# Kernel optimization log

Measured on AMD Instinct MI355X. Metric: run time of the kernel, lower is better.

Reference implementation:

```python
import jax, jax.numpy as jnp
import numpy as np

D_MODEL, D_STATE, D_CONV, EXPAND, L = 512, 16, 4, 2, 2048
D_INNER = EXPAND * D_MODEL


def _dwconv_causal(x, w, b):
    # x: (L, D), w: (D, K), b: (D,). torch Conv1d(groups=D, padding=K-1)[..., :L]
    K = w.shape[1]
    xp = jnp.pad(x, ((K - 1, 0), (0, 0)))
    windows = jnp.stack([xp[k:k + x.shape[0]] for k in range(K)], axis=-1)  # (L, D, K)
    return jnp.einsum('ldk,dk->ld', windows, w) + b


def _ssm_dir(x, inW, inb, cw, cb, xpW, xpb, dtW, dtb, outW, outb, A_log, Dp):
    xz = x @ inW + inb                      # (L, 2*Di)
    x_ssm, z = xz[:, :D_INNER], xz[:, D_INNER:]
    x_ssm = _dwconv_causal(x_ssm, cw, cb)   # (L, Di)
    sp = jax.nn.silu(x_ssm) @ xpW + xpb     # (L, Di + 2*S)
    delta = sp[:, :D_INNER]
    B = sp[:, D_INNER:D_INNER + D_STATE]
    C = sp[:, D_INNER + D_STATE:]
    dt = jax.nn.softplus(delta @ dtW + dtb)  # (L, Di)
    A = -jnp.exp(A_log)                      # (Di, S)
    dA = jnp.exp(dt[:, :, None] * A[None])                      # (L, Di, S)
    dBu = dt[:, :, None] * B[:, None, :] * x_ssm[:, :, None]    # (L, Di, S)

    def step(h, inp):
        a, bu = inp
        h = a * h + bu
        return h, h

    h0 = jnp.zeros((D_INNER, D_STATE), x.dtype)
    _, hs = jax.lax.scan(step, h0, (dA, dBu))   # (L, Di, S)
    y = jnp.einsum('lds,ls->ld', hs, C) + Dp * x_ssm
    return (y * jax.nn.silu(z)) @ outW + outb


def _make_params(key):
    ks = jax.random.split(key, 32)
    i = iter(range(32))
    def w(shape, scale=0.02):
        return (jax.random.normal(ks[next(i)], shape, jnp.float32) * scale)
    p = {}
    for pre in ('fwd_', 'bwd_'):
        p[pre + 'in_W'] = w((D_MODEL, 2 * D_INNER))
        p[pre + 'in_b'] = w((2 * D_INNER,))
        p[pre + 'conv_w'] = w((D_INNER, D_CONV), 0.1)
        p[pre + 'conv_b'] = w((D_INNER,))
        p[pre + 'xp_W'] = w((D_INNER, D_INNER + 2 * D_STATE))
        p[pre + 'xp_b'] = w((D_INNER + 2 * D_STATE,))
        p[pre + 'dt_W'] = w((D_INNER, D_INNER))
        p[pre + 'dt_b'] = w((D_INNER,))
        p[pre + 'out_W'] = w((D_INNER, D_MODEL))
        p[pre + 'out_b'] = w((D_MODEL,))
    p['A_log'] = jax.random.normal(ks[next(i)], (D_INNER, D_STATE), jnp.float32) * 0.5
    p['D_param'] = jnp.ones((D_INNER,), jnp.float32)
    p['fusion_W'] = w((2 * D_MODEL, D_MODEL))
    p['fusion_b'] = w((D_MODEL,))
    return p


def setup_inputs() -> dict:
    key = jax.random.key(0)
    kx, kp = jax.random.split(key)
    inp = {'x': jax.random.normal(kx, (L, D_MODEL), jnp.float32)}
    inp.update(_make_params(kp))
    return inp


def reference(x,
              fwd_in_W, fwd_in_b, fwd_conv_w, fwd_conv_b, fwd_xp_W, fwd_xp_b,
              fwd_dt_W, fwd_dt_b, fwd_out_W, fwd_out_b,
              bwd_in_W, bwd_in_b, bwd_conv_w, bwd_conv_b, bwd_xp_W, bwd_xp_b,
              bwd_dt_W, bwd_dt_b, bwd_out_W, bwd_out_b,
              A_log, D_param, fusion_W, fusion_b):
    out_fwd = _ssm_dir(x, fwd_in_W, fwd_in_b, fwd_conv_w, fwd_conv_b,
                       fwd_xp_W, fwd_xp_b, fwd_dt_W, fwd_dt_b,
                       fwd_out_W, fwd_out_b, A_log, D_param)
    out_bwd = _ssm_dir(x[::-1], bwd_in_W, bwd_in_b, bwd_conv_w, bwd_conv_b,
                       bwd_xp_W, bwd_xp_b, bwd_dt_W, bwd_dt_b,
                       bwd_out_W, bwd_out_b, A_log, D_param)[::-1]
    return jnp.concatenate([out_fwd, out_bwd], axis=-1) @ fusion_W + fusion_b
```

## Files before the change

kernel.cpp:

```cpp
#include <hip/hip_runtime.h>
#include <cmath>

#define L_SEQ 2048
#define DM 512
#define DI 1024
#define DS 16
#define NSP 1056
#define NC 64
#define CL 32

typedef unsigned short ushortT;
typedef unsigned int u32;
typedef __attribute__((ext_vector_type(8))) short short8;
typedef __attribute__((ext_vector_type(4))) float float4_t;
typedef __attribute__((address_space(1))) u32 gu32;
typedef __attribute__((address_space(3))) u32 lu32;

__device__ __forceinline__ float sigm(float x) { return 1.0f / (1.0f + __expf(-x)); }

__device__ __forceinline__ ushortT f2bf(float f) {
    unsigned u = __float_as_uint(f);
    unsigned r = u + 0x7FFFu + ((u >> 16) & 1u);
    return (ushortT)(r >> 16);
}

__device__ __forceinline__ void gl2lds16(const ushortT* g, ushortT* l) {
    __builtin_amdgcn_global_load_lds((gu32*)g, (lu32*)l, 16, 0, 0);
}

struct WC {
    const float* src[9];
    ushortT* dst[9];
    int K[9], N[9], tN[9];
    int off[10];
};

__global__ __launch_bounds__(256) void wcvt_all(WC wc)
{
    __shared__ ushortT t[32][33];
    int b = blockIdx.x;
    int m = 0;
    while (b >= wc.off[m + 1]) ++m;
    int tl = b - wc.off[m];
    int n0 = (tl % wc.tN[m]) * 32;
    int k0 = (tl / wc.tN[m]) * 32;
    const float* W = wc.src[m];
    ushortT* Wt = wc.dst[m];
    int K = wc.K[m], N = wc.N[m];
    int tx = threadIdx.x & 31, ty = threadIdx.x >> 5;
    #pragma unroll
    for (int i = 0; i < 32; i += 8)
        t[ty + i][tx] = f2bf(W[(size_t)(k0 + ty + i) * N + n0 + tx]);
    __syncthreads();
    #pragma unroll
    for (int i = 0; i < 32; i += 8)
        Wt[(size_t)(n0 + ty + i) * K + k0 + tx] = t[tx][ty + i];
}

__global__ __launch_bounds__(256) void xcvt_k(const float* __restrict__ x,
                                              ushortT* __restrict__ xb, int n)
{
    int i = (blockIdx.x * 256 + threadIdx.x) * 4;
    if (i < n) {
        float4_t v = *(const float4_t*)(x + i);
        xb[i + 0] = f2bf(v[0]); xb[i + 1] = f2bf(v[1]);
        xb[i + 2] = f2bf(v[2]); xb[i + 3] = f2bf(v[3]);
    }
}

template<int BM, int BN>
__global__ __launch_bounds__(256, 2) void gemm_bf16(
    const ushortT* __restrict__ A, int lda, long long Astr, int revAmode,
    const ushortT* __restrict__ W, long long Wstr,
    const float* __restrict__ bias0, const float* __restrict__ bias1,
    float* __restrict__ Cf, int ldcf, long long Cfstr,
    ushortT* __restrict__ Cb, int ldcb, long long Cbstr, int Nbmax,
    int revCmode, int M, int N, int K, int epi)
{
    const int dir = blockIdx.z;
    A  += (size_t)dir * Astr;
    W  += (size_t)dir * Wstr;
    if (Cf) Cf += (size_t)dir * Cfstr;
    if (Cb) Cb += (size_t)dir * Cbstr;
    const float* bias = dir ? bias1 : bias0;
    const int revA = (revAmode == 2) ? dir : revAmode;
    const int revC = (revCmode == 2) ? dir : revCmode;

    constexpr int MI = BM / 32;
    constexpr int NI = BN / 32;
    constexpr int CA = BM / 64;
    constexpr int CB = BN / 64;

    __shared__ ushortT As[2][BM * 32];
    __shared__ ushortT Bs[2][BN * 32];

    const int tid  = threadIdx.x;
    const int wave = tid >> 6;
    const int lane = tid & 63;
    const int quad = lane >> 4;
    const int r    = lane & 15;
    const int wm   = (wave >> 1) * (BM / 2);
    const int wn   = (wave & 1) * (BN / 2);
    const int bm   = blockIdx.y * BM;
    const int bn   = blockIdx.x * BN;

    const int lrow = lane >> 2;
    const int lk   = (lane & 3) * 8;

    const ushortT* gA[CA];
    ushortT* lA[CA];
    #pragma unroll
    for (int c = 0; c < CA; ++c) {
        int row = bm + c * 64 + wave * 16 + lrow;
        if (revA) row = M - 1 - row;
        gA[c] = A + (size_t)row * lda + lk;
        lA[c] = &As[0][(c * 64 + wave * 16) * 32];
    }
    const ushortT* gB[CB];
    ushortT* lB[CB];
    #pragma unroll
    for (int c = 0; c < CB; ++c) {
        int row = bn + c * 64 + wave * 16 + lrow;
        if (row > N - 1) row = N - 1;
        gB[c] = W + (size_t)row * K + lk;
        lB[c] = &Bs[0][(c * 64 + wave * 16) * 32];
    }
    constexpr int ABUF = BM * 32;
    constexpr int BBUF = BN * 32;

    float4_t acc[MI][NI];
    #pragma unroll
    for (int i = 0; i < MI; ++i)
        #pragma unroll
        for (int j = 0; j < NI; ++j)
            acc[i][j] = (float4_t){0.f, 0.f, 0.f, 0.f};

    const int nsteps = K >> 5;

    #pragma unroll
    for (int c = 0; c < CA; ++c) gl2lds16(gA[c], lA[c]);
    #pragma unroll
    for (int c = 0; c < CB; ++c) gl2lds16(gB[c], lB[c]);

    for (int i = 0; i < nsteps; i += 2) {
        __syncthreads();
        {
            int kq = (i + 1) << 5;
            if (i + 1 < nsteps) {
                #pragma unroll
                for (int c = 0; c < CA; ++c) gl2lds16(gA[c] + kq, lA[c] + ABUF);
                #pragma unroll
                for (int c = 0; c < CB; ++c) gl2lds16(gB[c] + kq, lB[c] + BBUF);
            }
        }
        {
            short8 af[MI], bf[NI];
            #pragma unroll
            for (int mi = 0; mi < MI; ++mi)
                af[mi] = *(const short8*)&As[0][(wm + mi * 16 + r) * 32 + quad * 8];
            #pragma unroll
            for (int ni = 0; ni < NI; ++ni)
                bf[ni] = *(const short8*)&Bs[0][(wn + ni * 16 + r) * 32 + quad * 8];
            #pragma unroll
            for (int mi = 0; mi < MI; ++mi)
                #pragma unroll
                for (int ni = 0; ni < NI; ++ni)
                    acc[mi][ni] = __builtin_amdgcn_mfma_f32_16x16x32_bf16(
                        af[mi], bf[ni], acc[mi][ni], 0, 0, 0);
        }
        __syncthreads();
        {
            int kq = (i + 2) << 5;
            if (i + 2 < nsteps) {
                #pragma unroll
                for (int c = 0; c < CA; ++c) gl2lds16(gA[c] + kq, lA[c]);
                #pragma unroll
                for (int c = 0; c < CB; ++c) gl2lds16(gB[c] + kq, lB[c]);
            }
        }
        {
            short8 af[MI], bf[NI];
            #pragma unroll
            for (int mi = 0; mi < MI; ++mi)
                af[mi] = *(const short8*)&As[1][(wm + mi * 16 + r) * 32 + quad * 8];
            #pragma unroll
            for (int ni = 0; ni < NI; ++ni)
                bf[ni] = *(const short8*)&Bs[1][(wn + ni * 16 + r) * 32 + quad * 8];
            #pragma unroll
            for (int mi = 0; mi < MI; ++mi)
                #pragma unroll
                for (int ni = 0; ni < NI; ++ni)
                    acc[mi][ni] = __builtin_amdgcn_mfma_f32_16x16x32_bf16(
                        af[mi], bf[ni], acc[mi][ni], 0, 0, 0);
        }
    }

    #pragma unroll
    for (int mi = 0; mi < MI; ++mi) {
        int rowb = bm + wm + mi * 16 + quad * 4;
        #pragma unroll
        for (int ni = 0; ni < NI; ++ni) {
            int gn = bn + wn + ni * 16 + r;
            if (gn < N) {
                float bv = bias[gn];
                #pragma unroll
                for (int j = 0; j < 4; ++j) {
                    int orow = rowb + j;
                    if (revC) orow = M - 1 - orow;
                    float v = acc[mi][ni][j] + bv;
                    if (epi == 1) v = (v > 20.0f) ? v : log1pf(__expf(v));
                    if (Cf) Cf[(size_t)orow * ldcf + gn] = v;
                    if (Cb && gn < Nbmax) Cb[(size_t)orow * ldcb + gn] = f2bf(v);
                }
            }
        }
    }
}

__global__ __launch_bounds__(256) void conv_k(
    const float* __restrict__ XZ,
    const float* __restrict__ cw0, const float* __restrict__ cw1,
    const float* __restrict__ cb0, const float* __restrict__ cb1,
    float* __restrict__ XC, ushortT* __restrict__ SCb)
{
    int dir = blockIdx.z;
    XZ += (size_t)dir * L_SEQ * 2 * DI;
    XC += (size_t)dir * L_SEQ * DI;
    SCb += (size_t)dir * L_SEQ * DI;
    const float* cw = dir ? cw1 : cw0;
    const float* cb = dir ? cb1 : cb0;
    int idx = blockIdx.x * 256 + threadIdx.x;
    int d = idx & (DI - 1);
    int l = idx >> 10;
    float w0 = cw[d * 4 + 0], w1 = cw[d * 4 + 1], w2 = cw[d * 4 + 2], w3 = cw[d * 4 + 3];
    float acc = cb[d];
    if (l >= 3) acc += XZ[(size_t)(l - 3) * (2 * DI) + d] * w0;
    if (l >= 2) acc += XZ[(size_t)(l - 2) * (2 * DI) + d] * w1;
    if (l >= 1) acc += XZ[(size_t)(l - 1) * (2 * DI) + d] * w2;
    acc += XZ[(size_t)l * (2 * DI) + d] * w3;
    XC[idx] = acc;
    SCb[idx] = f2bf(acc * sigm(acc));
}

__global__ __launch_bounds__(256) void scanA_k(
    const float* __restrict__ DT, const float* __restrict__ XC,
    const float* __restrict__ SP, const float* __restrict__ Alog,
    float* __restrict__ Pend, float* __restrict__ Hl)
{
    __shared__ float Bsh[CL][DS];
    int dir = blockIdx.z;
    int c = blockIdx.y;
    int d = blockIdx.x * 256 + threadIdx.x;
    DT += (size_t)dir * L_SEQ * DI;
    XC += (size_t)dir * L_SEQ * DI;
    SP += (size_t)dir * L_SEQ * NSP;
    int l0 = c * CL;
    for (int i = threadIdx.x; i < CL * DS; i += 256) {
        int ll = i >> 4, ss = i & 15;
        Bsh[ll][ss] = SP[(size_t)(l0 + ll) * NSP + DI + ss];
    }
    __syncthreads();
    float Ae[DS], h[DS], P[DS];
    #pragma unroll
    for (int s = 0; s < DS; ++s) { Ae[s] = -__expf(Alog[d * DS + s]); h[s] = 0.f; P[s] = 1.f; }
    for (int t = 0; t < CL; ++t) {
        int l = l0 + t;
        float dt = DT[(size_t)l * DI + d];
        float xv = XC[(size_t)l * DI + d];
        float dtx = dt * xv;
        #pragma unroll
        for (int s = 0; s < DS; ++s) {
            float e = __expf(dt * Ae[s]);
            h[s] = e * h[s] + dtx * Bsh[t][s];
            P[s] *= e;
        }
    }
    size_t o = ((size_t)(dir * NC + c) * DI + d) * DS;
    #pragma unroll
    for (int s = 0; s < DS; ++s) { Pend[o + s] = P[s]; Hl[o + s] = h[s]; }
}

__global__ __launch_bounds__(256) void scanB_k(
    const float* __restrict__ Pend, const float* __restrict__ Hl, float* __restrict__ Hs)
{
    int idx = blockIdx.x * 256 + threadIdx.x;
    float h = 0.f;
    int ds = idx & 16383;
    int dir = idx >> 14;
    for (int c = 0; c < NC; ++c) {
        size_t o = ((size_t)(dir * NC + c)) * (DI * DS) + ds;
        Hs[o] = h;
        h = Pend[o] * h + Hl[o];
    }
}

__global__ __launch_bounds__(256) void scanC_k(
    const float* __restrict__ DT, const float* __restrict__ XC,
    const float* __restrict__ SP, const float* __restrict__ XZ,
    const float* __restrict__ Alog, const float* __restrict__ Dp,
    const float* __restrict__ Hs, ushortT* __restrict__ Gb)
{
    __shared__ float Bsh[CL][DS];
    __shared__ float Csh[CL][DS];
    int dir = blockIdx.z;
    int c = blockIdx.y;
    int d = blockIdx.x * 256 + threadIdx.x;
    DT += (size_t)dir * L_SEQ * DI;
    XC += (size_t)dir * L_SEQ * DI;
    SP += (size_t)dir * L_SEQ * NSP;
    XZ += (size_t)dir * L_SEQ * (2 * DI);
    Gb += (size_t)dir * L_SEQ * DI;
    int l0 = c * CL;
    for (int i = threadIdx.x; i < CL * DS; i += 256) {
        int ll = i >> 4, ss = i & 15;
        size_t base = (size_t)(l0 + ll) * NSP + DI;
        Bsh[ll][ss] = SP[base + ss];
        Csh[ll][ss] = SP[base + DS + ss];
    }
    __syncthreads();
    float Ae[DS], h[DS];
    size_t o = ((size_t)(dir * NC + c) * DI + d) * DS;
    #pragma unroll
    for (int s = 0; s < DS; ++s) { Ae[s] = -__expf(Alog[d * DS + s]); h[s] = Hs[o + s]; }
    float dpv = Dp[d];
    for (int t = 0; t < CL; ++t) {
        int l = l0 + t;
        float dt = DT[(size_t)l * DI + d];
        float xv = XC[(size_t)l * DI + d];
        float dtx = dt * xv;
        float y = 0.f;
        #pragma unroll
        for (int s = 0; s < DS; ++s) {
            float e = __expf(dt * Ae[s]);
            h[s] = e * h[s] + dtx * Bsh[t][s];
            y += h[s] * Csh[t][s];
        }
        y += dpv * xv;
        float z = XZ[(size_t)l * (2 * DI) + DI + d];
        Gb[(size_t)l * DI + d] = f2bf(y * (z * sigm(z)));
    }
}

extern "C" void kernel_launch(void* const* d_in, const int* in_sizes, int n_in,
                              void* d_out, int out_size, void* d_ws, size_t ws_size,
                              hipStream_t stream)
{
    (void)in_sizes; (void)n_in; (void)out_size; (void)ws_size;
    const float* x = (const float*)d_in[0];
    const float* inW[2]  = {(const float*)d_in[1],  (const float*)d_in[11]};
    const float* inb[2]  = {(const float*)d_in[2],  (const float*)d_in[12]};
    const float* cw[2]   = {(const float*)d_in[3],  (const float*)d_in[13]};
    const float* cb[2]   = {(const float*)d_in[4],  (const float*)d_in[14]};
    const float* xpW[2]  = {(const float*)d_in[5],  (const float*)d_in[15]};
    const float* xpb[2]  = {(const float*)d_in[6],  (const float*)d_in[16]};
    const float* dtW[2]  = {(const float*)d_in[7],  (const float*)d_in[17]};
    const float* dtb[2]  = {(const float*)d_in[8],  (const float*)d_in[18]};
    const float* outW[2] = {(const float*)d_in[9],  (const float*)d_in[19]};
    const float* outb[2] = {(const float*)d_in[10], (const float*)d_in[20]};
    const float* Alog = (const float*)d_in[21];
    const float* Dp   = (const float*)d_in[22];
    const float* fuW  = (const float*)d_in[23];
    const float* fub  = (const float*)d_in[24];
    float* out = (float*)d_out;

    float* ws = (float*)d_ws;
    size_t off = 0;
    auto alloc = [&](size_t n) { float* p = ws + off; off += n; return p; };
    float* XZ  = alloc((size_t)2 * L_SEQ * 2 * DI);
    float* XC  = alloc((size_t)2 * L_SEQ * DI);
    float* SP  = alloc((size_t)2 * L_SEQ * NSP);
    float* DTb = alloc((size_t)2 * L_SEQ * DI);
    float* Pend= alloc((size_t)2 * NC * DI * DS);
    float* Hl  = alloc((size_t)2 * NC * DI * DS);
    float* Hs  = alloc((size_t)2 * NC * DI * DS);

    ushortT* wsu = (ushortT*)(ws + off);
    size_t uoff = 0;
    auto ualloc = [&](size_t n) { ushortT* p = wsu + uoff; uoff += n; return p; };
    ushortT* WtIn  = ualloc((size_t)2 * (2 * DI) * DM);
    ushortT* WtXp  = ualloc((size_t)2 * NSP * DI);
    ushortT* WtDt  = ualloc((size_t)2 * DI * DI);
    ushortT* WtOut = ualloc((size_t)2 * DM * DI);
    ushortT* WtFu  = ualloc((size_t)DM * DI);
    ushortT* XB    = ualloc((size_t)L_SEQ * DM);
    ushortT* SCb   = ualloc((size_t)2 * L_SEQ * DI);
    ushortT* SPb   = ualloc((size_t)2 * L_SEQ * DI);
    ushortT* Gb    = ualloc((size_t)2 * L_SEQ * DI);
    ushortT* OCb   = ualloc((size_t)L_SEQ * DI);

    dim3 blk(256);

    WC wc;
    const float* srcs[9] = {inW[0], inW[1], xpW[0], xpW[1], dtW[0], dtW[1],
                            outW[0], outW[1], fuW};
    ushortT* dsts[9] = {WtIn, WtIn + (size_t)2 * DI * DM,
                        WtXp, WtXp + (size_t)NSP * DI,
                        WtDt, WtDt + (size_t)DI * DI,
                        WtOut, WtOut + (size_t)DM * DI,
                        WtFu};
    int Ks[9] = {DM, DM, DI, DI, DI, DI, DI, DI, DI};
    int Ns[9] = {2 * DI, 2 * DI, NSP, NSP, DI, DI, DM, DM, DM};
    wc.off[0] = 0;
    for (int m = 0; m < 9; ++m) {
        wc.src[m] = srcs[m]; wc.dst[m] = dsts[m];
        wc.K[m] = Ks[m]; wc.N[m] = Ns[m];
        wc.tN[m] = Ns[m] / 32;
        wc.off[m + 1] = wc.off[m] + (Ns[m] / 32) * (Ks[m] / 32);
    }
    wcvt_all<<<dim3(wc.off[9]), blk, 0, stream>>>(wc);
    xcvt_k<<<dim3(L_SEQ * DM / 1024), blk, 0, stream>>>(x, XB, L_SEQ * DM);

    gemm_bf16<128, 128><<<dim3(16, 16, 2), blk, 0, stream>>>(
        XB, DM, 0, 2, WtIn, (long long)2 * DI * DM, inb[0], inb[1],
        XZ, 2 * DI, (long long)L_SEQ * 2 * DI, nullptr, 0, 0, 0,
        0, L_SEQ, 2 * DI, DM, 0);
    conv_k<<<dim3(L_SEQ * DI / 256, 1, 2), blk, 0, stream>>>(
        XZ, cw[0], cw[1], cb[0], cb[1], XC, SCb);
    gemm_bf16<128, 64><<<dim3((NSP + 63) / 64, 16, 2), blk, 0, stream>>>(
        SCb, DI, (long long)L_SEQ * DI, 0, WtXp, (long long)NSP * DI, xpb[0], xpb[1],
        SP, NSP, (long long)L_SEQ * NSP, SPb, DI, (long long)L_SEQ * DI, DI,
        0, L_SEQ, NSP, DI, 0);
    gemm_bf16<128, 64><<<dim3(16, 16, 2), blk, 0, stream>>>(
        SPb, DI, (long long)L_SEQ * DI, 0, WtDt, (long long)DI * DI, dtb[0], dtb[1],
        DTb, DI, (long long)L_SEQ * DI, nullptr, 0, 0, 0,
        0, L_SEQ, DI, DI, 1);
    scanA_k<<<dim3(DI / 256, NC, 2), blk, 0, stream>>>(DTb, XC, SP, Alog, Pend, Hl);
    scanB_k<<<dim3(2 * DI * DS / 256), blk, 0, stream>>>(Pend, Hl, Hs);
    scanC_k<<<dim3(DI / 256, NC, 2), blk, 0, stream>>>(DTb, XC, SP, XZ, Alog, Dp, Hs, Gb);
    gemm_bf16<64, 64><<<dim3(8, 32, 2), blk, 0, stream>>>(
        Gb, DI, (long long)L_SEQ * DI, 0, WtOut, (long long)DM * DI, outb[0], outb[1],
        nullptr, 0, 0, OCb, DI, (long long)DM, DM,
        2, L_SEQ, DM, DI, 0);
    gemm_bf16<64, 64><<<dim3(8, 32, 1), blk, 0, stream>>>(
        OCb, DI, 0, 0, WtFu, 0, fub, fub,
        out, DM, (long long)0, nullptr, 0, 0, 0,
        0, L_SEQ, DM, DI, 0);
}
```

Measured before the change: 346.8 us.

## Fold xp→dt and out→fusion weight products into precomputed combined GEMMs

Precomputes fused weight matrices (xp_W[:, :Di] @ dt_W, and out_W @ fusion_W halves) with small on-device GEMMs, plus folded biases. The separate dt projection GEMM and the fusion GEMM are removed from the main path: a single GEMM now produces softplus(dt) and B/C together, and the out projection accumulates both directions straight into the output with atomics after a memset. This cuts two large activation GEMMs and intermediate buffers, at the cost of extra weight-prep GEMMs per call, atomic contention, and altered bf16 rounding of combined weights. Tile sizes also change for the input GEMM and launch bounds are relaxed.

```diff
diff --git a/kernel.cpp b/kernel.cpp
--- a/kernel.cpp
+++ b/kernel.cpp
@@ -29,10 +29,10 @@
 }
 
 struct WC {
-    const float* src[9];
-    ushortT* dst[9];
-    int K[9], N[9], tN[9];
-    int off[10];
+    const float* src[11];
+    ushortT* dst[11];
+    int ss[11], soff[11], ds_[11], tN[11], mode[11];
+    int off[12];
 };
 
 __global__ __launch_bounds__(256) void wcvt_all(WC wc)
@@ -45,16 +45,55 @@
     int n0 = (tl % wc.tN[m]) * 32;
     int k0 = (tl / wc.tN[m]) * 32;
     const float* W = wc.src[m];
-    ushortT* Wt = wc.dst[m];
-    int K = wc.K[m], N = wc.N[m];
+    ushortT* D = wc.dst[m];
+    int ss = wc.ss[m], soff = wc.soff[m], ds = wc.ds_[m];
     int tx = threadIdx.x & 31, ty = threadIdx.x >> 5;
-    #pragma unroll
-    for (int i = 0; i < 32; i += 8)
-        t[ty + i][tx] = f2bf(W[(size_t)(k0 + ty + i) * N + n0 + tx]);
-    __syncthreads();
-    #pragma unroll
-    for (int i = 0; i < 32; i += 8)
-        Wt[(size_t)(n0 + ty + i) * K + k0 + tx] = t[tx][ty + i];
+    if (wc.mode[m] == 1) {
+        #pragma unroll
+        for (int i = 0; i < 32; i += 8)
+            D[(size_t)(k0 + ty + i) * ds + n0 + tx] =
+                f2bf(W[(size_t)(k0 + ty + i) * ss + soff + n0 + tx]);
+    } else {
+        #pragma unroll
+        for (int i = 0; i < 32; i += 8)
+            t[ty + i][tx] = f2bf(W[(size_t)(k0 + ty + i) * ss + soff + n0 + tx]);
+        __syncthreads();
+        #pragma unroll
+        for (int i = 0; i < 32; i += 8)
+            D[(size_t)(n0 + ty + i) * ds + k0 + tx] = t[tx][ty + i];
+    }
+}
+
+__global__ __launch_bounds__(256) void bias_fold(
+    const float* __restrict__ xpb0, const float* __restrict__ xpb1,
+    const float* __restrict__ dtW0, const float* __restrict__ dtW1,
+    const float* __restrict__ dtb0, const float* __restrict__ dtb1,
+    const float* __restrict__ outb0, const float* __restrict__ outb1,
+    const float* __restrict__ fuW, const float* __restrict__ fub,
+    float* __restrict__ BFdt0, float* __restrict__ BFdt1, float* __restrict__ BFof)
+{
+    int idx = blockIdx.x * 256 + threadIdx.x;
+    if (idx < 2112) {
+        int dir = idx >= 1056;
+        int m = idx - dir * 1056;
+        const float* xpb = dir ? xpb1 : xpb0;
+        float* BF = dir ? BFdt1 : BFdt0;
+        if (m < 1024) {
+            const float* dtW = dir ? dtW1 : dtW0;
+            const float* dtb = dir ? dtb1 : dtb0;
+            float acc = dtb[m];
+            for (int n = 0; n < 1024; ++n) acc += xpb[n] * dtW[n * 1024 + m];
+            BF[m] = acc;
+        } else {
+            BF[m] = xpb[m];
+        }
+    } else if (idx < 2624) {
+        int n = idx - 2112;
+        float acc = fub[n];
+        for (int j = 0; j < 512; ++j)  acc += outb0[j] * fuW[j * 512 + n];
+        for (int j = 0; j < 512; ++j)  acc += outb1[j] * fuW[(512 + j) * 512 + n];
+        BFof[n] = acc;
+    }
 }
 
 __global__ __launch_bounds__(256) void xcvt_k(const float* __restrict__ x,
@@ -69,22 +108,23 @@
 }
 
 template<int BM, int BN>
-__global__ __launch_bounds__(256, 2) void gemm_bf16(
+__global__ __launch_bounds__(256) void gemm_bf16(
     const ushortT* __restrict__ A, int lda, long long Astr, int revAmode,
     const ushortT* __restrict__ W, long long Wstr,
     const float* __restrict__ bias0, const float* __restrict__ bias1,
     float* __restrict__ Cf, int ldcf, long long Cfstr,
-    ushortT* __restrict__ Cb, int ldcb, long long Cbstr, int Nbmax,
-    int revCmode, int M, int N, int K, int epi)
+    float* __restrict__ Cf2, int ldcf2, long long Cf2str, int Nsplit,
+    ushortT* __restrict__ Cb, int ldcb, long long Cbstr,
+    int M, int N, int K, int epi)
 {
     const int dir = blockIdx.z;
     A  += (size_t)dir * Astr;
     W  += (size_t)dir * Wstr;
-    if (Cf) Cf += (size_t)dir * Cfstr;
-    if (Cb) Cb += (size_t)dir * Cbstr;
+    if (Cf)  Cf  += (size_t)dir * Cfstr;
+    if (Cf2) Cf2 += (size_t)dir * Cf2str;
+    if (Cb)  Cb  += (size_t)dir * Cbstr;
     const float* bias = dir ? bias1 : bias0;
     const int revA = (revAmode == 2) ? dir : revAmode;
-    const int revC = (revCmode == 2) ? dir : revCmode;
 
     constexpr int MI = BM / 32;
     constexpr int NI = BN / 32;
@@ -202,15 +242,22 @@
         for (int ni = 0; ni < NI; ++ni) {
             int gn = bn + wn + ni * 16 + r;
             if (gn < N) {
-                float bv = bias[gn];
+                float bv = bias ? bias[gn] : 0.0f;
                 #pragma unroll
                 for (int j = 0; j < 4; ++j) {
                     int orow = rowb + j;
-                    if (revC) orow = M - 1 - orow;
                     float v = acc[mi][ni][j] + bv;
-                    if (epi == 1) v = (v > 20.0f) ? v : log1pf(__expf(v));
-                    if (Cf) Cf[(size_t)orow * ldcf + gn] = v;
-                    if (Cb && gn < Nbmax) Cb[(size_t)orow * ldcb + gn] = f2bf(v);
+                    if (epi == 1 && gn < Nsplit) v = (v > 20.0f) ? v : log1pf(__expf(v));
+                    if (epi == 3) {
+                        atomicAdd(&Cf[(size_t)orow * ldcf + gn], v);
+                    } else {
+                        if (gn < Nsplit) {
+                            if (Cf) Cf[(size_t)orow * ldcf + gn] = v;
+                        } else if (Cf2) {
+                            Cf2[(size_t)orow * ldcf2 + gn - Nsplit] = v;
+                        }
+                        if (Cb) Cb[(size_t)orow * ldcb + gn] = f2bf(v);
+                    }
                 }
             }
         }
@@ -244,7 +291,7 @@
 
 __global__ __launch_bounds__(256) void scanA_k(
     const float* __restrict__ DT, const float* __restrict__ XC,
-    const float* __restrict__ SP, const float* __restrict__ Alog,
+    const float* __restrict__ BC, const float* __restrict__ Alog,
     float* __restrict__ Pend, float* __restrict__ Hl)
 {
     __shared__ float Bsh[CL][DS];
@@ -253,11 +300,11 @@
     int d = blockIdx.x * 256 + threadIdx.x;
     DT += (size_t)dir * L_SEQ * DI;
     XC += (size_t)dir * L_SEQ * DI;
-    SP += (size_t)dir * L_SEQ * NSP;
+    BC += (size_t)dir * L_SEQ * 32;
     int l0 = c * CL;
     for (int i = threadIdx.x; i < CL * DS; i += 256) {
         int ll = i >> 4, ss = i & 15;
-        Bsh[ll][ss] = SP[(size_t)(l0 + ll) * NSP + DI + ss];
+        Bsh[ll][ss] = BC[(size_t)(l0 + ll) * 32 + ss];
     }
     __syncthreads();
     float Ae[DS], h[DS], P[DS];
@@ -296,7 +343,7 @@
 
 __global__ __launch_bounds__(256) void scanC_k(
     const float* __restrict__ DT, const float* __restrict__ XC,
-    const float* __restrict__ SP, const float* __restrict__ XZ,
+    const float* __restrict__ BC, const float* __restrict__ XZ,
     const float* __restrict__ Alog, const float* __restrict__ Dp,
     const float* __restrict__ Hs, ushortT* __restrict__ Gb)
 {
@@ -307,15 +354,15 @@
     int d = blockIdx.x * 256 + threadIdx.x;
     DT += (size_t)dir * L_SEQ * DI;
     XC += (size_t)dir * L_SEQ * DI;
-    SP += (size_t)dir * L_SEQ * NSP;
+    BC += (size_t)dir * L_SEQ * 32;
     XZ += (size_t)dir * L_SEQ * (2 * DI);
     Gb += (size_t)dir * L_SEQ * DI;
     int l0 = c * CL;
     for (int i = threadIdx.x; i < CL * DS; i += 256) {
         int ll = i >> 4, ss = i & 15;
-        size_t base = (size_t)(l0 + ll) * NSP + DI;
-        Bsh[ll][ss] = SP[base + ss];
-        Csh[ll][ss] = SP[base + DS + ss];
+        size_t base = (size_t)(l0 + ll) * 32;
+        Bsh[ll][ss] = BC[base + ss];
+        Csh[ll][ss] = BC[base + DS + ss];
     }
     __syncthreads();
     float Ae[DS], h[DS];
@@ -366,73 +413,87 @@
     float* ws = (float*)d_ws;
     size_t off = 0;
     auto alloc = [&](size_t n) { float* p = ws + off; off += n; return p; };
-    float* XZ  = alloc((size_t)2 * L_SEQ * 2 * DI);
-    float* XC  = alloc((size_t)2 * L_SEQ * DI);
-    float* SP  = alloc((size_t)2 * L_SEQ * NSP);
-    float* DTb = alloc((size_t)2 * L_SEQ * DI);
-    float* Pend= alloc((size_t)2 * NC * DI * DS);
-    float* Hl  = alloc((size_t)2 * NC * DI * DS);
-    float* Hs  = alloc((size_t)2 * NC * DI * DS);
+    float* XZ   = alloc((size_t)2 * L_SEQ * 2 * DI);
+    float* XC   = alloc((size_t)2 * L_SEQ * DI);
+    float* DTb  = alloc((size_t)2 * L_SEQ * DI);
+    float* BCf  = alloc((size_t)2 * L_SEQ * 32);
+    float* Pend = alloc((size_t)2 * NC * DI * DS);
+    float* Hl   = alloc((size_t)2 * NC * DI * DS);
+    float* Hs   = alloc((size_t)2 * NC * DI * DS);
+    float* BFdt0 = alloc(1056);
+    float* BFdt1 = alloc(1056);
+    float* BFof  = alloc(512);
 
     ushortT* wsu = (ushortT*)(ws + off);
     size_t uoff = 0;
     auto ualloc = [&](size_t n) { ushortT* p = wsu + uoff; uoff += n; return p; };
     ushortT* WtIn  = ualloc((size_t)2 * (2 * DI) * DM);
-    ushortT* WtXp  = ualloc((size_t)2 * NSP * DI);
     ushortT* WtDt  = ualloc((size_t)2 * DI * DI);
-    ushortT* WtOut = ualloc((size_t)2 * DM * DI);
     ushortT* WtFu  = ualloc((size_t)DM * DI);
+    ushortT* WtXpF = ualloc((size_t)2 * NSP * DI);
+    ushortT* XpD   = ualloc((size_t)2 * DI * DI);
+    ushortT* OutC  = ualloc((size_t)2 * DI * DM);
+    ushortT* WtOF  = ualloc((size_t)2 * DM * DI);
     ushortT* XB    = ualloc((size_t)L_SEQ * DM);
     ushortT* SCb   = ualloc((size_t)2 * L_SEQ * DI);
-    ushortT* SPb   = ualloc((size_t)2 * L_SEQ * DI);
     ushortT* Gb    = ualloc((size_t)2 * L_SEQ * DI);
-    ushortT* OCb   = ualloc((size_t)L_SEQ * DI);
 
     dim3 blk(256);
 
+    hipMemsetAsync(out, 0, (size_t)L_SEQ * DM * sizeof(float), stream);
+
     WC wc;
-    const float* srcs[9] = {inW[0], inW[1], xpW[0], xpW[1], dtW[0], dtW[1],
-                            outW[0], outW[1], fuW};
-    ushortT* dsts[9] = {WtIn, WtIn + (size_t)2 * DI * DM,
-                        WtXp, WtXp + (size_t)NSP * DI,
-                        WtDt, WtDt + (size_t)DI * DI,
-                        WtOut, WtOut + (size_t)DM * DI,
-                        WtFu};
-    int Ks[9] = {DM, DM, DI, DI, DI, DI, DI, DI, DI};
-    int Ns[9] = {2 * DI, 2 * DI, NSP, NSP, DI, DI, DM, DM, DM};
+    struct E { const float* s; ushortT* d; int ss, so, ds, N, K, mode; };
+    E es[11] = {
+        {inW[0],  WtIn,                          2 * DI, 0,    DM, 2 * DI, DM, 0},
+        {inW[1],  WtIn + (size_t)2 * DI * DM,    2 * DI, 0,    DM, 2 * DI, DM, 0},
+        {dtW[0],  WtDt,                          DI,     0,    DI, DI,     DI, 0},
+        {dtW[1],  WtDt + (size_t)DI * DI,        DI,     0,    DI, DI,     DI, 0},
+        {fuW,     WtFu,                          DM,     0,    DI, DM,     DI, 0},
+        {xpW[0],  WtXpF + (size_t)DI * DI,       NSP,    DI,   DI, 32,     DI, 0},
+        {xpW[1],  WtXpF + (size_t)NSP * DI + (size_t)DI * DI, NSP, DI, DI, 32, DI, 0},
+        {xpW[0],  XpD,                           NSP,    0,    DI, DI,     DI, 1},
+        {xpW[1],  XpD + (size_t)DI * DI,         NSP,    0,    DI, DI,     DI, 1},
+        {outW[0], OutC,                          DM,     0,    DM, DM,     DI, 1},
+        {outW[1], OutC + (size_t)DI * DM,        DM,     0,    DM, DM,     DI, 1},
+    };
     wc.off[0] = 0;
-    for (int m = 0; m < 9; ++m) {
-        wc.src[m] = srcs[m]; wc.dst[m] = dsts[m];
-        wc.K[m] = Ks[m]; wc.N[m] = Ns[m];
-        wc.tN[m] = Ns[m] / 32;
-        wc.off[m + 1] = wc.off[m] + (Ns[m] / 32) * (Ks[m] / 32);
-    }
-    wcvt_all<<<dim3(wc.off[9]), blk, 0, stream>>>(wc);
+    for (int m = 0; m < 11; ++m) {
+        wc.src[m] = es[m].s; wc.dst[m] = es[m].d;
+        wc.ss[m] = es[m].ss; wc.soff[m] = es[m].so; wc.ds_[m] = es[m].ds;
+        wc.tN[m] = es[m].N / 32; wc.mode[m] = es[m].mode;
+        wc.off[m + 1] = wc.off[m] + (es[m].N / 32) * (es[m].K / 32);
+    }
+    wcvt_all<<<dim3(wc.off[11]), blk, 0, stream>>>(wc);
     xcvt_k<<<dim3(L_SEQ * DM / 1024), blk, 0, stream>>>(x, XB, L_SEQ * DM);
-
-    gemm_bf16<128, 128><<<dim3(16, 16, 2), blk, 0, stream>>>(
+    bias_fold<<<dim3(11), blk, 0, stream>>>(
+        xpb[0], xpb[1], dtW[0], dtW[1], dtb[0], dtb[1],
+        outb[0], outb[1], fuW, fub, BFdt0, BFdt1, BFof);
+
+    gemm_bf16<64, 64><<<dim3(16, 16, 2), blk, 0, stream>>>(
+        WtDt, DI, (long long)DI * DI, 0, XpD, (long long)DI * DI,
+        nullptr, nullptr, nullptr, 0, 0, nullptr, 0, 0, DI,
+        WtXpF, DI, (long long)NSP * DI, DI, DI, DI, 0);
+    gemm_bf16<64, 64><<<dim3(16, 8, 2), blk, 0, stream>>>(
+        WtFu, DI, (long long)DM, 0, OutC, (long long)DI * DM,
+        nullptr, nullptr, nullptr, 0, 0, nullptr, 0, 0, DI,
+        WtOF, DI, (long long)DM * DI, DM, DI, DM, 0);
+
+    gemm_bf16<64, 128><<<dim3(16, 32, 2), blk, 0, stream>>>(
         XB, DM, 0, 2, WtIn, (long long)2 * DI * DM, inb[0], inb[1],
-        XZ, 2 * DI, (long long)L_SEQ * 2 * DI, nullptr, 0, 0, 0,
-        0, L_SEQ, 2 * DI, DM, 0);
+        XZ, 2 * DI, (long long)L_SEQ * 2 * DI, nullptr, 0, 0, 2 * DI,
+        nullptr, 0, 0, L_SEQ, 2 * DI, DM, 0);
     conv_k<<<dim3(L_SEQ * DI / 256, 1, 2), blk, 0, stream>>>(
         XZ, cw[0], cw[1], cb[0], cb[1], XC, SCb);
-    gemm_bf16<128, 64><<<dim3((NSP + 63) / 64, 16, 2), blk, 0, stream>>>(
-        SCb, DI, (long long)L_SEQ * DI, 0, WtXp, (long long)NSP * DI, xpb[0], xpb[1],
-        SP, NSP, (long long)L_SEQ * NSP, SPb, DI, (long long)L_SEQ * DI, DI,
-        0, L_SEQ, NSP, DI, 0);
-    gemm_bf16<128, 64><<<dim3(16, 16, 2), blk, 0, stream>>>(
-        SPb, DI, (long long)L_SEQ * DI, 0, WtDt, (long long)DI * DI, dtb[0], dtb[1],
-        DTb, DI, (long long)L_SEQ * DI, nullptr, 0, 0, 0,
-        0, L_SEQ, DI, DI, 1);
-    scanA_k<<<dim3(DI / 256, NC, 2), blk, 0, stream>>>(DTb, XC, SP, Alog, Pend, Hl);
+    gemm_bf16<64, 64><<<dim3((NSP + 63) / 64, 32, 2), blk, 0, stream>>>(
+        SCb, DI, (long long)L_SEQ * DI, 0, WtXpF, (long long)NSP * DI, BFdt0, BFdt1,
+        DTb, DI, (long long)L_SEQ * DI, BCf, 32, (long long)L_SEQ * 32, DI,
+        nullptr, 0, 0, L_SEQ, NSP, DI, 1);
+    scanA_k<<<dim3(DI / 256, NC, 2), blk, 0, stream>>>(DTb, XC, BCf, Alog, Pend, Hl);
     scanB_k<<<dim3(2 * DI * DS / 256), blk, 0, stream>>>(Pend, Hl, Hs);
-    scanC_k<<<dim3(DI / 256, NC, 2), blk, 0, stream>>>(DTb, XC, SP, XZ, Alog, Dp, Hs, Gb);
-    gemm_bf16<64, 64><<<dim3(8, 32, 2), blk, 0, stream>>>(
-        Gb, DI, (long long)L_SEQ * DI, 0, WtOut, (long long)DM * DI, outb[0], outb[1],
-        nullptr, 0, 0, OCb, DI, (long long)DM, DM,
-        2, L_SEQ, DM, DI, 0);
-    gemm_bf16<64, 64><<<dim3(8, 32, 1), blk, 0, stream>>>(
-        OCb, DI, 0, 0, WtFu, 0, fub, fub,
-        out, DM, (long long)0, nullptr, 0, 0, 0,
-        0, L_SEQ, DM, DI, 0);
-}
+    scanC_k<<<dim3(DI / 256, NC, 2), blk, 0, stream>>>(DTb, XC, BCf, XZ, Alog, Dp, Hs, Gb);
+    gemm_bf16<64, 64><<<dim3(DM / 64, 32, 2), blk, 0, stream>>>(
+        Gb, DI, (long long)L_SEQ * DI, 2, WtOF, (long long)DM * DI, BFof, nullptr,
+        out, DM, 0, nullptr, 0, 0, DM,
+        nullptr, 0, 0, L_SEQ, DM, DI, 3);
+}
```

Result: slower. 374.3 us (+7.9%).
